# Kernel optimization log

Hardware: AMD Instinct MI355X
Metric: run time of the kernel (lower is better)

The kernel has to match this reference:

```python
import jax, jax.numpy as jnp
import numpy as np

N = 50000
E = 600000
HIDDEN = 128
HEADS = 4
HEAD_DIM = HIDDEN // HEADS
NEG_SLOPE = 0.2
LN_EPS = 1e-5


def setup_inputs() -> dict:
    key = jax.random.key(0)
    ks = jax.random.split(key, 16)
    s = 1.0 / np.sqrt(HIDDEN)
    inp = {
        "h": jax.random.normal(ks[0], (N, HIDDEN), dtype=jnp.float32),
        "src": jax.random.randint(ks[1], (E,), 0, N, dtype=jnp.int32),
        "dst": jax.random.randint(ks[2], (E,), 0, N, dtype=jnp.int32),
        # GATv2 params (share_weights=False, bias=True)
        "W_src": jax.random.normal(ks[3], (HIDDEN, HIDDEN), dtype=jnp.float32) * s,
        "b_src": jnp.zeros((HIDDEN,), dtype=jnp.float32),
        "W_dst": jax.random.normal(ks[4], (HIDDEN, HIDDEN), dtype=jnp.float32) * s,
        "b_dst": jnp.zeros((HIDDEN,), dtype=jnp.float32),
        "attn": jax.random.normal(ks[5], (HEADS, HEAD_DIM), dtype=jnp.float32) * s,
        # FFN params
        "W1": jax.random.normal(ks[6], (HIDDEN, 2 * HIDDEN), dtype=jnp.float32) * s,
        "bf1": jnp.zeros((2 * HIDDEN,), dtype=jnp.float32),
        "W2": jax.random.normal(ks[7], (2 * HIDDEN, HIDDEN), dtype=jnp.float32) * (1.0 / np.sqrt(2 * HIDDEN)),
        "bf2": jnp.zeros((HIDDEN,), dtype=jnp.float32),
        # LayerNorms
        "g1": jnp.ones((HIDDEN,), dtype=jnp.float32),
        "beta1": jnp.zeros((HIDDEN,), dtype=jnp.float32),
        "g2": jnp.ones((HIDDEN,), dtype=jnp.float32),
        "beta2": jnp.zeros((HIDDEN,), dtype=jnp.float32),
    }
    return inp


def _layernorm(x, g, b):
    mu = jnp.mean(x, axis=-1, keepdims=True)
    var = jnp.mean(jnp.square(x - mu), axis=-1, keepdims=True)
    return (x - mu) * jax.lax.rsqrt(var + LN_EPS) * g + b


def reference(h, src, dst, W_src, b_src, W_dst, b_dst, attn,
              W1, bf1, W2, bf2, g1, beta1, g2, beta2):
    # --- GATv2 attention (eval mode, dropouts are identity) ---
    fs = (h @ W_src + b_src).reshape(N, HEADS, HEAD_DIM)   # [N,H,D]
    fd = (h @ W_dst + b_dst).reshape(N, HEADS, HEAD_DIM)
    e = jax.nn.leaky_relu(fs[src] + fd[dst], NEG_SLOPE)    # [E,H,D]
    logits = jnp.einsum('ehd,hd->eh', e, attn)             # [E,H]
    # edge softmax over incoming edges of each dst node
    m = jax.ops.segment_max(logits, dst, num_segments=N)   # [N,H]
    m = jnp.where(jnp.isfinite(m), m, 0.0)                 # guard zero-in-degree
    a = jnp.exp(logits - m[dst])                           # [E,H]
    denom = jax.ops.segment_sum(a, dst, num_segments=N)    # [N,H]
    denom = jnp.where(denom == 0.0, 1.0, denom)
    alpha = a / denom[dst]                                 # [E,H]
    msg = fs[src] * alpha[:, :, None]                      # [E,H,D]
    rst = jax.ops.segment_sum(msg, dst, num_segments=N)    # [N,H,D]
    h_attn = rst.reshape(N, HIDDEN)
    # --- residual + LN, FFN + residual + LN ---
    h1 = _layernorm(h + h_attn, g1, beta1)
    ffn = jax.nn.gelu(h1 @ W1 + bf1, approximate=False) @ W2 + bf2
    out = _layernorm(h1 + ffn, g2, beta2)
    return out
```

## Files before the change

kernel.cpp:

```cpp
#include <hip/hip_runtime.h>
#include <math.h>

#define N_NODES 50000
#define N_EDGES 600000
#define HID 128
#define FFN_HID 256
#define NEG_SLOPE 0.2f
#define LN_EPS 1e-5f
#define BKT 64

typedef unsigned short u16;
typedef unsigned int u32;
typedef __attribute__((ext_vector_type(8))) short short8;
typedef __attribute__((ext_vector_type(4))) float floatx4;

__device__ __forceinline__ u16 f2bf(float x) {
    unsigned int u = __float_as_uint(x);
    unsigned int r = u + 0x7FFFu + ((u >> 16) & 1u);
    return (u16)(r >> 16);
}
__device__ __forceinline__ float bflo(u32 u) { return __uint_as_float(u << 16); }
__device__ __forceinline__ float bfhi(u32 u) { return __uint_as_float(u & 0xffff0000u); }
__device__ __forceinline__ u32 packbf(float lo, float hi) {
    return (u32)f2bf(lo) | ((u32)f2bf(hi) << 16);
}
__device__ __forceinline__ float gelu_fast(float v) {
    float u = 1.5957691216057308f * fmaf(0.044715f * v * v, v, v);
    return v / (1.0f + __expf(-u));
}


__global__ void scatter_prep(const int* __restrict__ src, const int* __restrict__ dst,
                             int* __restrict__ cursor, u16* __restrict__ ebkt,
                             const float* __restrict__ Wsrc, const float* __restrict__ Wdst,
                             const float* __restrict__ W1, const float* __restrict__ W2,
                             u16* __restrict__ B1, u16* __restrict__ B2, u16* __restrict__ B3) {
    int b = blockIdx.x;
    if (b < 2344) {
        int e = b * 256 + threadIdx.x;
        if (e < N_EDGES) {
            int d = dst[e];
            int slot = atomicAdd(&cursor[d], 1);
            if (slot < BKT) ebkt[(size_t)d * BKT + slot] = (u16)src[e];
        }
        return;
    }
    int t = (b - 2344) * 256 + threadIdx.x;
    const float* W; u16* out; int K, Nc, noff;
    if (t < 16384)       { W = Wsrc; out = B1; K = 128; Nc = 128; noff = 0; }
    else if (t < 32768)  { W = Wdst; out = B1; K = 128; Nc = 128; noff = 128; t -= 16384; }
    else if (t < 65536)  { W = W1;   out = B2; K = 128; Nc = 256; noff = 0;   t -= 32768; }
    else if (t < 98304)  { W = W2;   out = B3; K = 256; Nc = 128; noff = 0;   t -= 65536; }
    else return;
    int n = t % Nc, k = t / Nc;
    int ng = noff + n;
    int ksteps = K >> 5;
    int frag = (ng >> 4) * ksteps + (k >> 5);
    int lane = ((k >> 3) & 3) * 16 + (ng & 15);
    int j = k & 7;
    out[((size_t)frag * 64 + lane) * 8 + j] = f2bf(W[(size_t)k * Nc + n]);
}


__global__ __launch_bounds__(256) void gemm_fsfd_mfma(
    const float* __restrict__ h, const u16* __restrict__ Bsw,
    const float* __restrict__ bsrc, const float* __restrict__ bdst,
    u16* __restrict__ fsb, float* __restrict__ fdf)
{
    int tid = threadIdx.x, wave = tid >> 6, lane = tid & 63;
    int lrow = lane & 15, lq = lane >> 4;
    short8 bfrag[4][4];
    #pragma unroll
    for (int nt = 0; nt < 4; nt++)
        #pragma unroll
        for (int ks = 0; ks < 4; ks++) {
            int frag = (wave * 4 + nt) * 4 + ks;
            bfrag[nt][ks] = *(const short8*)(Bsw + ((size_t)frag * 64 + lane) * 8);
        }
    float bias[4];
    #pragma unroll
    for (int nt = 0; nt < 4; nt++) {
        int cg = wave * 64 + nt * 16 + lrow;
        bias[nt] = (cg < HID) ? bsrc[cg] : bdst[cg - HID];
    }
    for (int mb = blockIdx.x; mb < N_NODES / 16; mb += gridDim.x) {
        int m0 = mb * 16;
        const float* hrow = h + (size_t)(m0 + lrow) * HID;
        floatx4 acc[4];
        #pragma unroll
        for (int nt = 0; nt < 4; nt++) acc[nt] = {0.f, 0.f, 0.f, 0.f};
        #pragma unroll
        for (int ks = 0; ks < 4; ks++) {
            float4 va = *(const float4*)(hrow + ks * 32 + lq * 8);
            float4 vb = *(const float4*)(hrow + ks * 32 + lq * 8 + 4);
            short8 a;
            a[0] = (short)f2bf(va.x); a[1] = (short)f2bf(va.y);
            a[2] = (short)f2bf(va.z); a[3] = (short)f2bf(va.w);
            a[4] = (short)f2bf(vb.x); a[5] = (short)f2bf(vb.y);
            a[6] = (short)f2bf(vb.z); a[7] = (short)f2bf(vb.w);
            #pragma unroll
            for (int nt = 0; nt < 4; nt++)
                acc[nt] = __builtin_amdgcn_mfma_f32_16x16x32_bf16(a, bfrag[nt][ks], acc[nt], 0, 0, 0);
        }
        #pragma unroll
        for (int nt = 0; nt < 4; nt++) {
            int cg = wave * 64 + nt * 16 + lrow;
            if (cg < HID) {
                #pragma unroll
                for (int r = 0; r < 4; r++) {
                    int row = m0 + lq * 4 + r;
                    fsb[(size_t)row * HID + cg] = f2bf(acc[nt][r] + bias[nt]);
                }
            } else {
                #pragma unroll
                for (int r = 0; r < 4; r++) {
                    int row = m0 + lq * 4 + r;
                    fdf[(size_t)row * HID + cg - HID] = acc[nt][r] + bias[nt];
                }
            }
        }
    }
}


__global__ __launch_bounds__(256) void aggregate_kernel(
    const u16* __restrict__ fsb, const float* __restrict__ fdf,
    const float* __restrict__ h, const float* __restrict__ attn,
    const int* __restrict__ counts, const u16* __restrict__ ebkt,
    const float* __restrict__ g1, const float* __restrict__ beta1,
    float* __restrict__ h1f, u16* __restrict__ h1b)
{
    int wave = threadIdx.x >> 6, lane = threadIdx.x & 63;
    int node = blockIdx.x * 4 + wave;
    if (node >= N_NODES) return;
    int grp = lane >> 4, fl = lane & 15;
    int f = fl * 8;

    float4 d0 = *(const float4*)&fdf[(size_t)node * HID + f];
    float4 d1 = *(const float4*)&fdf[(size_t)node * HID + f + 4];
    float fdv[8] = { d0.x, d0.y, d0.z, d0.w, d1.x, d1.y, d1.z, d1.w };
    float4 aA = *(const float4*)&attn[f];
    float4 aB = *(const float4*)&attn[f + 4];
    float c1[8] = { 0.6f * aA.x, 0.6f * aA.y, 0.6f * aA.z, 0.6f * aA.w,
                    0.6f * aB.x, 0.6f * aB.y, 0.6f * aB.z, 0.6f * aB.w };
    float c2[8] = { 0.4f * aA.x, 0.4f * aA.y, 0.4f * aA.z, 0.4f * aA.w,
                    0.4f * aB.x, 0.4f * aB.y, 0.4f * aB.z, 0.4f * aB.w };

    int cnt = counts[node]; cnt = cnt < BKT ? cnt : BKT;
    const u16* brow = ebkt + (size_t)node * BKT;
    float acc[8] = {0.f, 0.f, 0.f, 0.f, 0.f, 0.f, 0.f, 0.f};
    float lsum = 0.f;

    auto body = [&](int e) {
        int s = (int)brow[e];
        uint4 u = *(const uint4*)&fsb[(size_t)s * HID + f];
        float x[8] = { bflo(u.x), bfhi(u.x), bflo(u.y), bfhi(u.y),
                       bflo(u.z), bfhi(u.z), bflo(u.w), bfhi(u.w) };
        float p = 0.f;
        #pragma unroll
        for (int i = 0; i < 8; i++) {
            float ei = x[i] + fdv[i];
            p = fmaf(c1[i], ei, p);
            p = fmaf(c2[i], fabsf(ei), p);
        }
        p += __shfl_xor(p, 1); p += __shfl_xor(p, 2);
        float w = __expf(p);
        lsum += w;
        #pragma unroll
        for (int i = 0; i < 8; i++) acc[i] = fmaf(w, x[i], acc[i]);
    };

    int e = grp;
    for (; e + 4 < cnt; e += 8) { body(e); body(e + 4); }
    if (e < cnt) body(e);

    #pragma unroll
    for (int i = 0; i < 8; i++) {
        acc[i] += __shfl_xor(acc[i], 16);
        acc[i] += __shfl_xor(acc[i], 32);
    }
    lsum += __shfl_xor(lsum, 16); lsum += __shfl_xor(lsum, 32);

    float inv = (lsum > 0.f) ? (1.0f / lsum) : 0.f;
    float4 h0 = *(const float4*)&h[(size_t)node * HID + f];
    float4 h1v = *(const float4*)&h[(size_t)node * HID + f + 4];
    float hx[8] = { h0.x, h0.y, h0.z, h0.w, h1v.x, h1v.y, h1v.z, h1v.w };
    float o[8], s1 = 0.f, s2 = 0.f;
    #pragma unroll
    for (int i = 0; i < 8; i++) {
        o[i] = hx[i] + acc[i] * inv;
        s1 += o[i]; s2 += o[i] * o[i];
    }
    s1 += __shfl_xor(s1, 1); s2 += __shfl_xor(s2, 1);
    s1 += __shfl_xor(s1, 2); s2 += __shfl_xor(s2, 2);
    s1 += __shfl_xor(s1, 4); s2 += __shfl_xor(s2, 4);
    s1 += __shfl_xor(s1, 8); s2 += __shfl_xor(s2, 8);
    float mu = s1 * (1.0f / HID);
    float var = s2 * (1.0f / HID) - mu * mu;
    float rs = rsqrtf(var + LN_EPS);
    if (grp == 0) {
        float4 gA = *(const float4*)&g1[f], gB = *(const float4*)&g1[f + 4];
        float4 bA = *(const float4*)&beta1[f], bB = *(const float4*)&beta1[f + 4];
        float q0 = (o[0] - mu) * rs * gA.x + bA.x, q1 = (o[1] - mu) * rs * gA.y + bA.y;
        float q2 = (o[2] - mu) * rs * gA.z + bA.z, q3 = (o[3] - mu) * rs * gA.w + bA.w;
        float q4 = (o[4] - mu) * rs * gB.x + bB.x, q5 = (o[5] - mu) * rs * gB.y + bB.y;
        float q6 = (o[6] - mu) * rs * gB.z + bB.z, q7 = (o[7] - mu) * rs * gB.w + bB.w;
        *(float4*)&h1f[(size_t)node * HID + f]     = make_float4(q0, q1, q2, q3);
        *(float4*)&h1f[(size_t)node * HID + f + 4] = make_float4(q4, q5, q6, q7);
        uint4 ob;
        ob.x = packbf(q0, q1); ob.y = packbf(q2, q3);
        ob.z = packbf(q4, q5); ob.w = packbf(q6, q7);
        *(uint4*)&h1b[(size_t)node * HID + f] = ob;
    }
}


#define FF_TILES (N_NODES / 16)

__global__ __launch_bounds__(256) void ffn1_kernel(
    const u16* __restrict__ h1b, const u16* __restrict__ B2sw,
    const float* __restrict__ bf1, u16* __restrict__ tbuf)
{
    __shared__ u16 bs[32768];
    for (int i = threadIdx.x; i < 4096; i += 256)
        *(uint4*)(bs + (size_t)i * 8) = *(const uint4*)(B2sw + (size_t)i * 8);
    __syncthreads();
    int wave = threadIdx.x >> 6, lane = threadIdx.x & 63;
    int lrow = lane & 15, lq = lane >> 4;
    int tile = blockIdx.x * 4 + wave;
    if (tile >= FF_TILES) return;
    int m0 = tile * 16;

    floatx4 acc[16];
    #pragma unroll
    for (int nt = 0; nt < 16; nt++) acc[nt] = {0.f, 0.f, 0.f, 0.f};
    #pragma unroll
    for (int ks = 0; ks < 4; ks++) {
        short8 a = *(const short8*)(h1b + (size_t)(m0 + lrow) * HID + ks * 32 + lq * 8);
        #pragma unroll
        for (int nt = 0; nt < 16; nt++) {
            short8 b = *(const short8*)&bs[((nt * 4 + ks) * 64 + lane) * 8];
            acc[nt] = __builtin_amdgcn_mfma_f32_16x16x32_bf16(a, b, acc[nt], 0, 0, 0);
        }
    }
    #pragma unroll
    for (int nt = 0; nt < 16; nt++) {
        float bias = bf1[nt * 16 + lrow];
        #pragma unroll
        for (int r = 0; r < 4; r++) {
            float v = acc[nt][r] + bias;
            tbuf[(size_t)(m0 + lq * 4 + r) * FFN_HID + nt * 16 + lrow] = f2bf(gelu_fast(v));
        }
    }
}

__global__ __launch_bounds__(256) void ffn2_kernel(
    const u16* __restrict__ tbuf, const float* __restrict__ h1f,
    const u16* __restrict__ B3sw, const float* __restrict__ bf2,
    const float* __restrict__ g2, const float* __restrict__ beta2,
    float* __restrict__ out)
{
    __shared__ u16 bs[32768];
    for (int i = threadIdx.x; i < 4096; i += 256)
        *(uint4*)(bs + (size_t)i * 8) = *(const uint4*)(B3sw + (size_t)i * 8);
    __syncthreads();
    int wave = threadIdx.x >> 6, lane = threadIdx.x & 63;
    int lrow = lane & 15, lq = lane >> 4;
    int tile = blockIdx.x * 4 + wave;
    if (tile >= FF_TILES) return;
    int m0 = tile * 16;

    floatx4 acc[8];
    #pragma unroll
    for (int nt = 0; nt < 8; nt++) acc[nt] = {0.f, 0.f, 0.f, 0.f};
    #pragma unroll
    for (int ks = 0; ks < 8; ks++) {
        short8 a = *(const short8*)(tbuf + (size_t)(m0 + lrow) * FFN_HID + ks * 32 + lq * 8);
        #pragma unroll
        for (int nt = 0; nt < 8; nt++) {
            short8 b = *(const short8*)&bs[((nt * 8 + ks) * 64 + lane) * 8];
            acc[nt] = __builtin_amdgcn_mfma_f32_16x16x32_bf16(a, b, acc[nt], 0, 0, 0);
        }
    }
    float xv[8][4];
    #pragma unroll
    for (int nt = 0; nt < 8; nt++) {
        float bias = bf2[nt * 16 + lrow];
        #pragma unroll
        for (int r = 0; r < 4; r++) {
            int row = m0 + lq * 4 + r;
            xv[nt][r] = acc[nt][r] + bias + h1f[(size_t)row * HID + nt * 16 + lrow];
        }
    }
    #pragma unroll
    for (int r = 0; r < 4; r++) {
        float s1 = 0.f, s2 = 0.f;
        #pragma unroll
        for (int nt = 0; nt < 8; nt++) { s1 += xv[nt][r]; s2 += xv[nt][r] * xv[nt][r]; }
        s1 += __shfl_xor(s1, 1); s2 += __shfl_xor(s2, 1);
        s1 += __shfl_xor(s1, 2); s2 += __shfl_xor(s2, 2);
        s1 += __shfl_xor(s1, 4); s2 += __shfl_xor(s2, 4);
        s1 += __shfl_xor(s1, 8); s2 += __shfl_xor(s2, 8);
        float mu = s1 * (1.0f / HID);
        float var = s2 * (1.0f / HID) - mu * mu;
        float rstd = rsqrtf(var + LN_EPS);
        int row = m0 + lq * 4 + r;
        #pragma unroll
        for (int nt = 0; nt < 8; nt++) {
            int cg = nt * 16 + lrow;
            out[(size_t)row * HID + cg] = (xv[nt][r] - mu) * rstd * g2[cg] + beta2[cg];
        }
    }
}


extern "C" void kernel_launch(void* const* d_in, const int* in_sizes, int n_in,
                              void* d_out, int out_size, void* d_ws, size_t ws_size,
                              hipStream_t stream)
{
    const float* h    = (const float*)d_in[0];
    const int*   src  = (const int*)d_in[1];
    const int*   dst  = (const int*)d_in[2];
    const float* Wsrc = (const float*)d_in[3];
    const float* bsrc = (const float*)d_in[4];
    const float* Wdst = (const float*)d_in[5];
    const float* bdst = (const float*)d_in[6];
    const float* attn = (const float*)d_in[7];
    const float* W1   = (const float*)d_in[8];
    const float* bf1  = (const float*)d_in[9];
    const float* W2   = (const float*)d_in[10];
    const float* bf2  = (const float*)d_in[11];
    const float* g1   = (const float*)d_in[12];
    const float* beta1= (const float*)d_in[13];
    const float* g2   = (const float*)d_in[14];
    const float* beta2= (const float*)d_in[15];
    float* out = (float*)d_out;

    u16* fsb = (u16*)d_ws;
    float* fdf = (float*)(fsb + (size_t)N_NODES * HID);
    float* h1f = fdf + (size_t)N_NODES * HID;
    u16* h1b = (u16*)(h1f + (size_t)N_NODES * HID);
    u16* B1 = h1b + (size_t)N_NODES * HID;
    u16* B2 = B1 + 32768;
    u16* B3 = B2 + 32768;
    int* cursor = (int*)(B3 + 32768);
    u16* ebkt   = (u16*)(cursor + N_NODES);
    u16* tbuf   = (u16*)fdf;

    hipMemsetAsync(cursor, 0, N_NODES * sizeof(int), stream);
    scatter_prep<<<2728, 256, 0, stream>>>(src, dst, cursor, ebkt,
                                           Wsrc, Wdst, W1, W2, B1, B2, B3);
    gemm_fsfd_mfma<<<1024, 256, 0, stream>>>(h, B1, bsrc, bdst, fsb, fdf);
    aggregate_kernel<<<(N_NODES + 3) / 4, 256, 0, stream>>>(fsb, fdf, h, attn, cursor, ebkt, g1, beta1, h1f, h1b);
    ffn1_kernel<<<(FF_TILES + 3) / 4, 256, 0, stream>>>(h1b, B2, bf1, tbuf);
    ffn2_kernel<<<(FF_TILES + 3) / 4, 256, 0, stream>>>(tbuf, h1f, B3, bf2, g2, beta2, out);
}
```

Before: 252.4 us.

## Store fd in bf16 and make the GEMM kernels persistent with LDS-staged weights

The fs/fd projection GEMM now stages the whole swizzled weight matrix in shared memory. Each wave computes all 256 output columns for a 16-row tile, so every h row is read and converted once instead of by each wave. fd is stored as bf16 rather than fp32, which halves its write and read traffic at some precision cost in the attention logits. The FFN kernels become grid-stride persistent loops with 391 blocks, so the weight load into LDS is amortised over several tiles, and the bias and LayerNorm parameters are hoisted into registers. tbuf now aliases fsb, which is free once aggregation has finished.

New measurement: 258.7 us. 1.02x slower.

```diff
diff --git a/kernel.cpp b/kernel.cpp
--- a/kernel.cpp
+++ b/kernel.cpp
@@ -28,6 +28,8 @@
     float u = 1.5957691216057308f * fmaf(0.044715f * v * v, v, v);
     return v / (1.0f + __expf(-u));
 }
+
+#define FF_TILES (N_NODES / 16)
 
 
 __global__ void scatter_prep(const int* __restrict__ src, const int* __restrict__ dst,
@@ -65,30 +67,25 @@
 __global__ __launch_bounds__(256) void gemm_fsfd_mfma(
     const float* __restrict__ h, const u16* __restrict__ Bsw,
     const float* __restrict__ bsrc, const float* __restrict__ bdst,
-    u16* __restrict__ fsb, float* __restrict__ fdf)
-{
-    int tid = threadIdx.x, wave = tid >> 6, lane = tid & 63;
+    u16* __restrict__ fsb, u16* __restrict__ fdb)
+{
+    __shared__ u16 bs[32768];
+    for (int i = threadIdx.x; i < 4096; i += 256)
+        *(uint4*)(bs + (size_t)i * 8) = *(const uint4*)(Bsw + (size_t)i * 8);
+    __syncthreads();
+    int wave = threadIdx.x >> 6, lane = threadIdx.x & 63;
     int lrow = lane & 15, lq = lane >> 4;
-    short8 bfrag[4][4];
-    #pragma unroll
-    for (int nt = 0; nt < 4; nt++)
-        #pragma unroll
-        for (int ks = 0; ks < 4; ks++) {
-            int frag = (wave * 4 + nt) * 4 + ks;
-            bfrag[nt][ks] = *(const short8*)(Bsw + ((size_t)frag * 64 + lane) * 8);
-        }
-    float bias[4];
-    #pragma unroll
-    for (int nt = 0; nt < 4; nt++) {
-        int cg = wave * 64 + nt * 16 + lrow;
-        bias[nt] = (cg < HID) ? bsrc[cg] : bdst[cg - HID];
-    }
-    for (int mb = blockIdx.x; mb < N_NODES / 16; mb += gridDim.x) {
-        int m0 = mb * 16;
+    float bias[16];
+    #pragma unroll
+    for (int nt = 0; nt < 16; nt++)
+        bias[nt] = (nt < 8) ? bsrc[nt * 16 + lrow] : bdst[(nt - 8) * 16 + lrow];
+
+    for (int tile = blockIdx.x * 4 + wave; tile < FF_TILES; tile += gridDim.x * 4) {
+        int m0 = tile * 16;
         const float* hrow = h + (size_t)(m0 + lrow) * HID;
-        floatx4 acc[4];
-        #pragma unroll
-        for (int nt = 0; nt < 4; nt++) acc[nt] = {0.f, 0.f, 0.f, 0.f};
+        floatx4 acc[16];
+        #pragma unroll
+        for (int nt = 0; nt < 16; nt++) acc[nt] = {0.f, 0.f, 0.f, 0.f};
         #pragma unroll
         for (int ks = 0; ks < 4; ks++) {
             float4 va = *(const float4*)(hrow + ks * 32 + lq * 8);
@@ -99,24 +96,19 @@
             a[4] = (short)f2bf(vb.x); a[5] = (short)f2bf(vb.y);
             a[6] = (short)f2bf(vb.z); a[7] = (short)f2bf(vb.w);
             #pragma unroll
-            for (int nt = 0; nt < 4; nt++)
-                acc[nt] = __builtin_amdgcn_mfma_f32_16x16x32_bf16(a, bfrag[nt][ks], acc[nt], 0, 0, 0);
-        }
-        #pragma unroll
-        for (int nt = 0; nt < 4; nt++) {
-            int cg = wave * 64 + nt * 16 + lrow;
-            if (cg < HID) {
-                #pragma unroll
-                for (int r = 0; r < 4; r++) {
-                    int row = m0 + lq * 4 + r;
-                    fsb[(size_t)row * HID + cg] = f2bf(acc[nt][r] + bias[nt]);
-                }
-            } else {
-                #pragma unroll
-                for (int r = 0; r < 4; r++) {
-                    int row = m0 + lq * 4 + r;
-                    fdf[(size_t)row * HID + cg - HID] = acc[nt][r] + bias[nt];
-                }
+            for (int nt = 0; nt < 16; nt++) {
+                short8 bfr = *(const short8*)&bs[((nt * 4 + ks) * 64 + lane) * 8];
+                acc[nt] = __builtin_amdgcn_mfma_f32_16x16x32_bf16(a, bfr, acc[nt], 0, 0, 0);
+            }
+        }
+        #pragma unroll
+        for (int nt = 0; nt < 16; nt++) {
+            u16* outp = (nt < 8) ? fsb : fdb;
+            int cg = (nt & 7) * 16 + lrow;
+            #pragma unroll
+            for (int r = 0; r < 4; r++) {
+                int row = m0 + lq * 4 + r;
+                outp[(size_t)row * HID + cg] = f2bf(acc[nt][r] + bias[nt]);
             }
         }
     }
@@ -124,7 +116,7 @@
 
 
 __global__ __launch_bounds__(256) void aggregate_kernel(
-    const u16* __restrict__ fsb, const float* __restrict__ fdf,
+    const u16* __restrict__ fsb, const u16* __restrict__ fdb,
     const float* __restrict__ h, const float* __restrict__ attn,
     const int* __restrict__ counts, const u16* __restrict__ ebkt,
     const float* __restrict__ g1, const float* __restrict__ beta1,
@@ -136,9 +128,9 @@
     int grp = lane >> 4, fl = lane & 15;
     int f = fl * 8;
 
-    float4 d0 = *(const float4*)&fdf[(size_t)node * HID + f];
-    float4 d1 = *(const float4*)&fdf[(size_t)node * HID + f + 4];
-    float fdv[8] = { d0.x, d0.y, d0.z, d0.w, d1.x, d1.y, d1.z, d1.w };
+    uint4 ud = *(const uint4*)&fdb[(size_t)node * HID + f];
+    float fdv[8] = { bflo(ud.x), bfhi(ud.x), bflo(ud.y), bfhi(ud.y),
+                     bflo(ud.z), bfhi(ud.z), bflo(ud.w), bfhi(ud.w) };
     float4 aA = *(const float4*)&attn[f];
     float4 aB = *(const float4*)&attn[f + 4];
     float c1[8] = { 0.6f * aA.x, 0.6f * aA.y, 0.6f * aA.z, 0.6f * aA.w,
@@ -215,8 +207,6 @@
 }
 
 
-#define FF_TILES (N_NODES / 16)
-
 __global__ __launch_bounds__(256) void ffn1_kernel(
     const u16* __restrict__ h1b, const u16* __restrict__ B2sw,
     const float* __restrict__ bf1, u16* __restrict__ tbuf)
@@ -227,29 +217,31 @@
     __syncthreads();
     int wave = threadIdx.x >> 6, lane = threadIdx.x & 63;
     int lrow = lane & 15, lq = lane >> 4;
-    int tile = blockIdx.x * 4 + wave;
-    if (tile >= FF_TILES) return;
-    int m0 = tile * 16;
-
-    floatx4 acc[16];
-    #pragma unroll
-    for (int nt = 0; nt < 16; nt++) acc[nt] = {0.f, 0.f, 0.f, 0.f};
-    #pragma unroll
-    for (int ks = 0; ks < 4; ks++) {
-        short8 a = *(const short8*)(h1b + (size_t)(m0 + lrow) * HID + ks * 32 + lq * 8);
+    float bias[16];
+    #pragma unroll
+    for (int nt = 0; nt < 16; nt++) bias[nt] = bf1[nt * 16 + lrow];
+
+    for (int tile = blockIdx.x * 4 + wave; tile < FF_TILES; tile += gridDim.x * 4) {
+        int m0 = tile * 16;
+        floatx4 acc[16];
+        #pragma unroll
+        for (int nt = 0; nt < 16; nt++) acc[nt] = {0.f, 0.f, 0.f, 0.f};
+        #pragma unroll
+        for (int ks = 0; ks < 4; ks++) {
+            short8 a = *(const short8*)(h1b + (size_t)(m0 + lrow) * HID + ks * 32 + lq * 8);
+            #pragma unroll
+            for (int nt = 0; nt < 16; nt++) {
+                short8 b = *(const short8*)&bs[((nt * 4 + ks) * 64 + lane) * 8];
+                acc[nt] = __builtin_amdgcn_mfma_f32_16x16x32_bf16(a, b, acc[nt], 0, 0, 0);
+            }
+        }
         #pragma unroll
         for (int nt = 0; nt < 16; nt++) {
-            short8 b = *(const short8*)&bs[((nt * 4 + ks) * 64 + lane) * 8];
-            acc[nt] = __builtin_amdgcn_mfma_f32_16x16x32_bf16(a, b, acc[nt], 0, 0, 0);
-        }
-    }
-    #pragma unroll
-    for (int nt = 0; nt < 16; nt++) {
-        float bias = bf1[nt * 16 + lrow];
-        #pragma unroll
-        for (int r = 0; r < 4; r++) {
-            float v = acc[nt][r] + bias;
-            tbuf[(size_t)(m0 + lq * 4 + r) * FFN_HID + nt * 16 + lrow] = f2bf(gelu_fast(v));
+            #pragma unroll
+            for (int r = 0; r < 4; r++) {
+                float v = acc[nt][r] + bias[nt];
+                tbuf[(size_t)(m0 + lq * 4 + r) * FFN_HID + nt * 16 + lrow] = f2bf(gelu_fast(v));
+            }
         }
     }
 }
@@ -266,49 +258,54 @@
     __syncthreads();
     int wave = threadIdx.x >> 6, lane = threadIdx.x & 63;
     int lrow = lane & 15, lq = lane >> 4;
-    int tile = blockIdx.x * 4 + wave;
-    if (tile >= FF_TILES) return;
-    int m0 = tile * 16;
-
-    floatx4 acc[8];
-    #pragma unroll
-    for (int nt = 0; nt < 8; nt++) acc[nt] = {0.f, 0.f, 0.f, 0.f};
-    #pragma unroll
-    for (int ks = 0; ks < 8; ks++) {
-        short8 a = *(const short8*)(tbuf + (size_t)(m0 + lrow) * FFN_HID + ks * 32 + lq * 8);
+    float bias2[8], g2v[8], be2v[8];
+    #pragma unroll
+    for (int nt = 0; nt < 8; nt++) {
+        int cg = nt * 16 + lrow;
+        bias2[nt] = bf2[cg]; g2v[nt] = g2[cg]; be2v[nt] = beta2[cg];
+    }
+
+    for (int tile = blockIdx.x * 4 + wave; tile < FF_TILES; tile += gridDim.x * 4) {
+        int m0 = tile * 16;
+        floatx4 acc[8];
+        #pragma unroll
+        for (int nt = 0; nt < 8; nt++) acc[nt] = {0.f, 0.f, 0.f, 0.f};
+        #pragma unroll
+        for (int ks = 0; ks < 8; ks++) {
+            short8 a = *(const short8*)(tbuf + (size_t)(m0 + lrow) * FFN_HID + ks * 32 + lq * 8);
+            #pragma unroll
+            for (int nt = 0; nt < 8; nt++) {
+                short8 b = *(const short8*)&bs[((nt * 8 + ks) * 64 + lane) * 8];
+                acc[nt] = __builtin_amdgcn_mfma_f32_16x16x32_bf16(a, b, acc[nt], 0, 0, 0);
+            }
+        }
+        float xv[8][4];
         #pragma unroll
         for (int nt = 0; nt < 8; nt++) {
-            short8 b = *(const short8*)&bs[((nt * 8 + ks) * 64 + lane) * 8];
-            acc[nt] = __builtin_amdgcn_mfma_f32_16x16x32_bf16(a, b, acc[nt], 0, 0, 0);
-        }
-    }
-    float xv[8][4];
-    #pragma unroll
-    for (int nt = 0; nt < 8; nt++) {
-        float bias = bf2[nt * 16 + lrow];
+            #pragma unroll
+            for (int r = 0; r < 4; r++) {
+                int row = m0 + lq * 4 + r;
+                xv[nt][r] = acc[nt][r] + bias2[nt] + h1f[(size_t)row * HID + nt * 16 + lrow];
+            }
+        }
         #pragma unroll
         for (int r = 0; r < 4; r++) {
+            float s1 = 0.f, s2 = 0.f;
+            #pragma unroll
+            for (int nt = 0; nt < 8; nt++) { s1 += xv[nt][r]; s2 += xv[nt][r] * xv[nt][r]; }
+            s1 += __shfl_xor(s1, 1); s2 += __shfl_xor(s2, 1);
+            s1 += __shfl_xor(s1, 2); s2 += __shfl_xor(s2, 2);
+            s1 += __shfl_xor(s1, 4); s2 += __shfl_xor(s2, 4);
+            s1 += __shfl_xor(s1, 8); s2 += __shfl_xor(s2, 8);
+            float mu = s1 * (1.0f / HID);
+            float var = s2 * (1.0f / HID) - mu * mu;
+            float rstd = rsqrtf(var + LN_EPS);
             int row = m0 + lq * 4 + r;
-            xv[nt][r] = acc[nt][r] + bias + h1f[(size_t)row * HID + nt * 16 + lrow];
-        }
-    }
-    #pragma unroll
-    for (int r = 0; r < 4; r++) {
-        float s1 = 0.f, s2 = 0.f;
-        #pragma unroll
-        for (int nt = 0; nt < 8; nt++) { s1 += xv[nt][r]; s2 += xv[nt][r] * xv[nt][r]; }
-        s1 += __shfl_xor(s1, 1); s2 += __shfl_xor(s2, 1);
-        s1 += __shfl_xor(s1, 2); s2 += __shfl_xor(s2, 2);
-        s1 += __shfl_xor(s1, 4); s2 += __shfl_xor(s2, 4);
-        s1 += __shfl_xor(s1, 8); s2 += __shfl_xor(s2, 8);
-        float mu = s1 * (1.0f / HID);
-        float var = s2 * (1.0f / HID) - mu * mu;
-        float rstd = rsqrtf(var + LN_EPS);
-        int row = m0 + lq * 4 + r;
-        #pragma unroll
-        for (int nt = 0; nt < 8; nt++) {
-            int cg = nt * 16 + lrow;
-            out[(size_t)row * HID + cg] = (xv[nt][r] - mu) * rstd * g2[cg] + beta2[cg];
+            #pragma unroll
+            for (int nt = 0; nt < 8; nt++) {
+                int cg = nt * 16 + lrow;
+                out[(size_t)row * HID + cg] = (xv[nt][r] - mu) * rstd * g2v[nt] + be2v[nt];
+            }
         }
     }
 }
@@ -337,21 +334,21 @@
     float* out = (float*)d_out;
 
     u16* fsb = (u16*)d_ws;
-    float* fdf = (float*)(fsb + (size_t)N_NODES * HID);
-    float* h1f = fdf + (size_t)N_NODES * HID;
+    u16* fdb = fsb + (size_t)N_NODES * HID;
+    float* h1f = (float*)(fdb + (size_t)N_NODES * HID);
     u16* h1b = (u16*)(h1f + (size_t)N_NODES * HID);
     u16* B1 = h1b + (size_t)N_NODES * HID;
     u16* B2 = B1 + 32768;
     u16* B3 = B2 + 32768;
     int* cursor = (int*)(B3 + 32768);
     u16* ebkt   = (u16*)(cursor + N_NODES);
-    u16* tbuf   = (u16*)fdf;
+    u16* tbuf   = fsb;
 
     hipMemsetAsync(cursor, 0, N_NODES * sizeof(int), stream);
     scatter_prep<<<2728, 256, 0, stream>>>(src, dst, cursor, ebkt,
                                            Wsrc, Wdst, W1, W2, B1, B2, B3);
-    gemm_fsfd_mfma<<<1024, 256, 0, stream>>>(h, B1, bsrc, bdst, fsb, fdf);
-    aggregate_kernel<<<(N_NODES + 3) / 4, 256, 0, stream>>>(fsb, fdf, h, attn, cursor, ebkt, g1, beta1, h1f, h1b);
-    ffn1_kernel<<<(FF_TILES + 3) / 4, 256, 0, stream>>>(h1b, B2, bf1, tbuf);
-    ffn2_kernel<<<(FF_TILES + 3) / 4, 256, 0, stream>>>(tbuf, h1f, B3, bf2, g2, beta2, out);
-}
+    gemm_fsfd_mfma<<<391, 256, 0, stream>>>(h, B1, bsrc, bdst, fsb, fdb);
+    aggregate_kernel<<<(N_NODES + 3) / 4, 256, 0, stream>>>(fsb, fdb, h, attn, cursor, ebkt, g1, beta1, h1f, h1b);
+    ffn1_kernel<<<391, 256, 0, stream>>>(h1b, B2, bf1, tbuf);
+    ffn2_kernel<<<391, 256, 0, stream>>>(tbuf, h1f, B3, bf2, g2, beta2, out);
+}
```
